# Optimization experiments

Hardware: AMD Instinct MI355X
Metric: run time of the kernel (lower is better)

Reference implementation:

```python
import jax, jax.numpy as jnp
import numpy as np

TEMPERATURE = 2.0  # exp(log(2.0)) clamped to [0.1, 10] -> 2.0
EPS = 1e-8
B, D, P = 2048, 256, 4


def setup_inputs() -> dict:
    key = jax.random.key(0)
    k1, k2, k3, k4 = jax.random.split(key, 4)
    return {
        'z_i': jax.random.normal(k1, (B, D), dtype=jnp.float32),
        'z_j': jax.random.normal(k2, (B, D), dtype=jnp.float32),
        'physics_i': jax.random.uniform(k3, (B, P), dtype=jnp.float32),
        'physics_j': jax.random.uniform(k4, (B, P), dtype=jnp.float32),
    }


def _offdiag(x, flat_idx, n):
    # extract off-diagonal entries of (n,n) -> (n, n-1), row-major order
    return jnp.take(x.reshape(-1), flat_idx).reshape(n, n - 1)


def reference(z_i, z_j, physics_i, physics_j):
    features = jnp.concatenate([z_i, z_j], axis=0)          # (n, D)
    labels = jnp.concatenate([physics_i, physics_j], axis=0)  # (n, P)
    n = features.shape[0]

    # pairwise L1 label distances (n, n)
    label_diffs = jnp.abs(labels[:, None, :] - labels[None, :, :]).sum(-1)

    # cosine similarity logits (n, n)
    f = features / jnp.linalg.norm(features, axis=-1, keepdims=True)
    logits = (f @ f.T) / TEMPERATURE
    logits = logits - jax.lax.stop_gradient(jnp.max(logits, axis=1, keepdims=True))
    exp_logits = jnp.exp(logits)

    flat_idx = jnp.asarray(np.flatnonzero(~np.eye(n, dtype=bool)))
    logits_o = _offdiag(logits, flat_idx, n)      # (n, n-1)
    exp_o = _offdiag(exp_logits, flat_idx, n)
    ld_o = _offdiag(label_diffs, flat_idx, n)

    # denom[i,k] = sum_j [ld_o[i,j] >= ld_o[i,k]] * exp_o[i,j]
    # computed via per-row sort + cumsum instead of the O(n^3) mask loop
    order = jnp.argsort(ld_o, axis=1)
    ld_sorted = jnp.take_along_axis(ld_o, order, axis=1)
    exp_sorted = jnp.take_along_axis(exp_o, order, axis=1)
    csum = jnp.cumsum(exp_sorted, axis=1)
    total = csum[:, -1:]
    # rank[i,k] = number of j with ld_o[i,j] < ld_o[i,k]  (side='left' handles ties)
    rank = jax.vmap(lambda s, q: jnp.searchsorted(s, q, side='left'))(ld_sorted, ld_o)
    below = jnp.where(rank > 0,
                      jnp.take_along_axis(csum, jnp.maximum(rank - 1, 0), axis=1),
                      0.0)
    denom = total - below                          # (n, n-1)

    pos_log_probs = logits_o - jnp.log(denom + EPS)
    loss = -pos_log_probs.sum() / (n * (n - 1))
    return loss
```

## Files before the change

kernel.cpp:

```cpp
#include <hip/hip_runtime.h>
#include <float.h>
#include <math.h>

#define B_SZ   2048
#define D_DIM  256
#define P_DIM  4
#define N_TOT  4096
#define EPS_F  1e-8f
#define RPP    16
#define NBK    512
#define BSCALE 128.0f
#define FIXS   1048576.0f

typedef float     f32x4 __attribute__((ext_vector_type(4)));
typedef long long i64;

__global__ __launch_bounds__(64) void normalize_kernel(
    const float* __restrict__ z_i, const float* __restrict__ z_j,
    unsigned char* __restrict__ fbq)
{
    int row  = blockIdx.x;
    int lane = threadIdx.x;
    const float* src = (row < B_SZ) ? (z_i + (size_t)row * D_DIM)
                                    : (z_j + (size_t)(row - B_SZ) * D_DIM);
    float4 v = ((const float4*)src)[lane];
    float ss = v.x*v.x + v.y*v.y + v.z*v.z + v.w*v.w;
    #pragma unroll
    for (int off = 32; off > 0; off >>= 1)
        ss += __shfl_down(ss, off, 64);
    ss = __shfl(ss, 0, 64);
    float inv = 1.0f / sqrtf(ss);
    int p = __builtin_amdgcn_cvt_pk_fp8_f32(v.x * inv, v.y * inv, 0, false);
    p     = __builtin_amdgcn_cvt_pk_fp8_f32(v.z * inv, v.w * inv, p, true);
    ((int*)(fbq + (size_t)row * D_DIM))[lane] = p;
}

__global__ __launch_bounds__(1024, 4) void panel_kernel(
    const unsigned char* __restrict__ fbq,
    const float* __restrict__ physics_i, const float* __restrict__ physics_j,
    float* __restrict__ partial)
{
    __shared__ unsigned long long hist[RPP * NBK];
    __shared__ float scr[16];

    int tid = threadIdx.x;
    int L   = tid & 63;
    int w   = tid >> 6;
    int i0  = blockIdx.x * RPP;

    uint4 zu = {0u, 0u, 0u, 0u};
    #pragma unroll
    for (int t = 0; t < 4; ++t)
        ((uint4*)hist)[tid + t * 1024] = zu;

    i64 a8[8];
    {
        const unsigned char* ap = fbq + (size_t)(i0 + (L & 15)) * D_DIM + (L >> 4) * 8;
        #pragma unroll
        for (int kc = 0; kc < 8; ++kc)
            a8[kc] = *(const i64*)(ap + kc * 32);
    }
    float4 Lr[4];
    #pragma unroll
    for (int q = 0; q < 4; ++q) {
        int r = i0 + (L >> 4) * 4 + q;
        const float* p = (r < B_SZ) ? physics_i + (size_t)r * P_DIM
                                    : physics_j + (size_t)(r - B_SZ) * P_DIM;
        Lr[q] = *(const float4*)p;
    }

    __syncthreads();

    #define LOADB(BB, LJ, ct)                                                     \
        {                                                                         \
            int jc_ = (ct) * 256 + w * 16 + (L & 15);                             \
            const unsigned char* bp_ = fbq + (size_t)jc_ * D_DIM + (L >> 4) * 8;  \
            _Pragma("unroll")                                                     \
            for (int kc = 0; kc < 8; ++kc)                                        \
                BB[kc] = *(const i64*)(bp_ + kc * 32);                            \
            const float* pj_ = (jc_ < B_SZ)                                       \
                ? physics_i + (size_t)jc_ * P_DIM                                 \
                : physics_j + (size_t)(jc_ - B_SZ) * P_DIM;                       \
            LJ = *(const float4*)pj_;                                             \
        }

    #define COMPUTE(BB, LJ, ct)                                                   \
        {                                                                         \
            int jc_ = (ct) * 256 + w * 16 + (L & 15);                             \
            f32x4 acc0 = {0.f, 0.f, 0.f, 0.f};                                    \
            f32x4 acc1 = {0.f, 0.f, 0.f, 0.f};                                    \
            _Pragma("unroll")                                                     \
            for (int kc = 0; kc < 4; ++kc) {                                      \
                acc0 = __builtin_amdgcn_mfma_f32_16x16x32_fp8_fp8(                \
                    a8[2*kc],   BB[2*kc],   acc0, 0, 0, 0);                       \
                acc1 = __builtin_amdgcn_mfma_f32_16x16x32_fp8_fp8(                \
                    a8[2*kc+1], BB[2*kc+1], acc1, 0, 0, 0);                       \
            }                                                                     \
            _Pragma("unroll")                                                     \
            for (int q = 0; q < 4; ++q) {                                         \
                int rq = (L >> 4) * 4 + q;                                        \
                float logit = (acc0[q] + acc1[q]) * 0.5f;              \
                float d = fabsf(Lr[q].x - LJ.x) + fabsf(Lr[q].y - LJ.y)           \
                        + fabsf(Lr[q].z - LJ.z) + fabsf(Lr[q].w - LJ.w);          \
                int bk = (int)(d * BSCALE); if (bk > NBK - 1) bk = NBK - 1;       \
                if (jc_ != i0 + rq) {                                             \
                    unsigned long long upd = (1ULL << 40)                         \
                        + (unsigned long long)(__expf(logit) * FIXS);             \
                    atomicAdd(&hist[rq * NBK + bk], upd);                         \
                    SL += logit;                                                  \
                }                                                                 \
            }                                                                     \
        }

    float SL = 0.f;
    i64    bA[8], bB[8];
    float4 LjA, LjB;
    LOADB(bA, LjA, 0)
    for (int ct = 0; ct < 16; ct += 2) {
        LOADB(bB, LjB, ct + 1)
        COMPUTE(bA, LjA, ct)
        if (ct + 2 < 16) LOADB(bA, LjA, ct + 2)
        COMPUTE(bB, LjB, ct + 1)
    }
    __syncthreads();

    float term = 0.f;
    {
        const unsigned long long* hr = hist + w * NBK + L * 8;
        float    v[8];
        unsigned c[8];
        float fs = 0.f;
        #pragma unroll
        for (int k = 0; k < 8; ++k) {
            unsigned long long x = hr[k];
            v[k] = (float)(x & 0xFFFFFFFFFFULL) * (1.0f / FIXS);
            c[k] = (unsigned)(x >> 40);
            fs += v[k];
        }
        float s = fs;
        #pragma unroll
        for (int off = 1; off < 64; off <<= 1) {
            float u = __shfl_down(s, off, 64);
            if (L + off < 64) s += u;
        }
        float run = s - fs;
        #pragma unroll
        for (int k = 7; k >= 0; --k) {
            run += v[k];
            if (c[k]) term += (float)c[k] * __logf(run + EPS_F);
        }
    }

    float acc = SL - term;
    #pragma unroll
    for (int off = 32; off > 0; off >>= 1)
        acc += __shfl_down(acc, off, 64);
    if (L == 0) scr[w] = acc;
    __syncthreads();
    if (tid == 0) {
        float s = 0.f;
        #pragma unroll
        for (int w2 = 0; w2 < 16; ++w2) s += scr[w2];
        partial[blockIdx.x] = s;
    }
    #undef LOADB
    #undef COMPUTE
}

__global__ __launch_bounds__(256) void final_kernel(
    const float* __restrict__ partial, float* __restrict__ out)
{
    __shared__ float red[4];
    int tid = threadIdx.x;
    float s = 0.f;
    for (int i = tid; i < N_TOT / RPP; i += 256) s += partial[i];
    #pragma unroll
    for (int off = 32; off > 0; off >>= 1)
        s += __shfl_down(s, off, 64);
    if ((tid & 63) == 0) red[tid >> 6] = s;
    __syncthreads();
    if (tid == 0) {
        double tot = (double)red[0] + red[1] + red[2] + red[3];
        out[0] = (float)(-tot / ((double)N_TOT * (N_TOT - 1)));
    }
}

extern "C" void kernel_launch(void* const* d_in, const int* in_sizes, int n_in,
                              void* d_out, int out_size, void* d_ws, size_t ws_size,
                              hipStream_t stream)
{
    const float* z_i  = (const float*)d_in[0];
    const float* z_j  = (const float*)d_in[1];
    const float* ph_i = (const float*)d_in[2];
    const float* ph_j = (const float*)d_in[3];

    unsigned char* fbq     = (unsigned char*)d_ws;
    float*         partial = (float*)(fbq + (size_t)N_TOT * D_DIM);

    normalize_kernel<<<N_TOT, 64, 0, stream>>>(z_i, z_j, fbq);
    panel_kernel<<<N_TOT / RPP, 1024, 0, stream>>>(fbq, ph_i, ph_j, partial);
    final_kernel<<<1, 256, 0, stream>>>(partial, (float*)d_out);
}
```

Before: 129.1 us.

## Use float LDS histogram and recompute logits in a second pass

The 64-bit fixed-point LDS histogram that packed counts and exp sums is replaced with a 32-bit float histogram updated by float atomics. The suffix sums are written back into the histogram, and a second full pass recomputes the MFMA logits and bucket indices so each pair can look up its denominator and accumulate logit minus log. This removes the 64-bit atomics and halves LDS use, at the cost of doubling the MFMA work and the global B-tile loads and of taking one log per pair instead of one per bucket.

```diff
diff --git a/kernel.cpp b/kernel.cpp
--- a/kernel.cpp
+++ b/kernel.cpp
@@ -10,7 +10,6 @@
 #define RPP    16
 #define NBK    512
 #define BSCALE 128.0f
-#define FIXS   1048576.0f
 
 typedef float     f32x4 __attribute__((ext_vector_type(4)));
 typedef long long i64;
@@ -40,7 +39,7 @@
     const float* __restrict__ physics_i, const float* __restrict__ physics_j,
     float* __restrict__ partial)
 {
-    __shared__ unsigned long long hist[RPP * NBK];
+    __shared__ float hist[RPP * NBK];
     __shared__ float scr[16];
 
     int tid = threadIdx.x;
@@ -48,10 +47,10 @@
     int w   = tid >> 6;
     int i0  = blockIdx.x * RPP;
 
-    uint4 zu = {0u, 0u, 0u, 0u};
-    #pragma unroll
-    for (int t = 0; t < 4; ++t)
-        ((uint4*)hist)[tid + t * 1024] = zu;
+    float4 z4 = {0.f, 0.f, 0.f, 0.f};
+    #pragma unroll
+    for (int t = 0; t < 2; ++t)
+        ((float4*)hist)[tid + t * 1024] = z4;
 
     i64 a8[8];
     {
@@ -84,9 +83,7 @@
             LJ = *(const float4*)pj_;                                             \
         }
 
-    #define COMPUTE(BB, LJ, ct)                                                   \
-        {                                                                         \
-            int jc_ = (ct) * 256 + w * 16 + (L & 15);                             \
+    #define MFMA8(BB)                                                             \
             f32x4 acc0 = {0.f, 0.f, 0.f, 0.f};                                    \
             f32x4 acc1 = {0.f, 0.f, 0.f, 0.f};                                    \
             _Pragma("unroll")                                                     \
@@ -95,7 +92,12 @@
                     a8[2*kc],   BB[2*kc],   acc0, 0, 0, 0);                       \
                 acc1 = __builtin_amdgcn_mfma_f32_16x16x32_fp8_fp8(                \
                     a8[2*kc+1], BB[2*kc+1], acc1, 0, 0, 0);                       \
-            }                                                                     \
+            }
+
+    #define COMPUTE_H(BB, LJ, ct)                                                 \
+        {                                                                         \
+            int jc_ = (ct) * 256 + w * 16 + (L & 15);                             \
+            MFMA8(BB)                                                             \
             _Pragma("unroll")                                                     \
             for (int q = 0; q < 4; ++q) {                                         \
                 int rq = (L >> 4) * 4 + q;                                        \
@@ -103,40 +105,46 @@
                 float d = fabsf(Lr[q].x - LJ.x) + fabsf(Lr[q].y - LJ.y)           \
                         + fabsf(Lr[q].z - LJ.z) + fabsf(Lr[q].w - LJ.w);          \
                 int bk = (int)(d * BSCALE); if (bk > NBK - 1) bk = NBK - 1;       \
-                if (jc_ != i0 + rq) {                                             \
-                    unsigned long long upd = (1ULL << 40)                         \
-                        + (unsigned long long)(__expf(logit) * FIXS);             \
-                    atomicAdd(&hist[rq * NBK + bk], upd);                         \
-                    SL += logit;                                                  \
-                }                                                                 \
+                if (jc_ != i0 + rq)                                               \
+                    atomicAdd(&hist[rq * NBK + bk], __expf(logit));               \
             }                                                                     \
         }
 
-    float SL = 0.f;
-    i64    bA[8], bB[8];
-    float4 LjA, LjB;
-    LOADB(bA, LjA, 0)
-    for (int ct = 0; ct < 16; ct += 2) {
-        LOADB(bB, LjB, ct + 1)
-        COMPUTE(bA, LjA, ct)
-        if (ct + 2 < 16) LOADB(bA, LjA, ct + 2)
-        COMPUTE(bB, LjB, ct + 1)
-    }
-    __syncthreads();
-
-    float term = 0.f;
-    {
-        const unsigned long long* hr = hist + w * NBK + L * 8;
-        float    v[8];
-        unsigned c[8];
+    #define COMPUTE_L(BB, LJ, ct)                                                 \
+        {                                                                         \
+            int jc_ = (ct) * 256 + w * 16 + (L & 15);                             \
+            MFMA8(BB)                                                             \
+            _Pragma("unroll")                                                     \
+            for (int q = 0; q < 4; ++q) {                                         \
+                int rq = (L >> 4) * 4 + q;                                        \
+                float logit = (acc0[q] + acc1[q]) * 0.5f;              \
+                float d = fabsf(Lr[q].x - LJ.x) + fabsf(Lr[q].y - LJ.y)           \
+                        + fabsf(Lr[q].z - LJ.z) + fabsf(Lr[q].w - LJ.w);          \
+                int bk = (int)(d * BSCALE); if (bk > NBK - 1) bk = NBK - 1;       \
+                if (jc_ != i0 + rq)                                               \
+                    ACC += logit - __logf(hist[rq * NBK + bk] + EPS_F);           \
+            }                                                                     \
+        }
+
+    {
+        i64    bA[8], bB[8];
+        float4 LjA, LjB;
+        LOADB(bA, LjA, 0)
+        for (int ct = 0; ct < 16; ct += 2) {
+            LOADB(bB, LjB, ct + 1)
+            COMPUTE_H(bA, LjA, ct)
+            if (ct + 2 < 16) LOADB(bA, LjA, ct + 2)
+            COMPUTE_H(bB, LjB, ct + 1)
+        }
+    }
+    __syncthreads();
+
+    {
+        float* hrow = hist + w * NBK + L * 8;
+        float v[8];
         float fs = 0.f;
         #pragma unroll
-        for (int k = 0; k < 8; ++k) {
-            unsigned long long x = hr[k];
-            v[k] = (float)(x & 0xFFFFFFFFFFULL) * (1.0f / FIXS);
-            c[k] = (unsigned)(x >> 40);
-            fs += v[k];
-        }
+        for (int k = 0; k < 8; ++k) { v[k] = hrow[k]; fs += v[k]; }
         float s = fs;
         #pragma unroll
         for (int off = 1; off < 64; off <<= 1) {
@@ -145,17 +153,27 @@
         }
         float run = s - fs;
         #pragma unroll
-        for (int k = 7; k >= 0; --k) {
-            run += v[k];
-            if (c[k]) term += (float)c[k] * __logf(run + EPS_F);
-        }
-    }
-
-    float acc = SL - term;
+        for (int k = 7; k >= 0; --k) { run += v[k]; hrow[k] = run; }
+    }
+    __syncthreads();
+
+    float ACC = 0.f;
+    {
+        i64    bA[8], bB[8];
+        float4 LjA, LjB;
+        LOADB(bA, LjA, 0)
+        for (int ct = 0; ct < 16; ct += 2) {
+            LOADB(bB, LjB, ct + 1)
+            COMPUTE_L(bA, LjA, ct)
+            if (ct + 2 < 16) LOADB(bA, LjA, ct + 2)
+            COMPUTE_L(bB, LjB, ct + 1)
+        }
+    }
+
     #pragma unroll
     for (int off = 32; off > 0; off >>= 1)
-        acc += __shfl_down(acc, off, 64);
-    if (L == 0) scr[w] = acc;
+        ACC += __shfl_down(ACC, off, 64);
+    if (L == 0) scr[w] = ACC;
     __syncthreads();
     if (tid == 0) {
         float s = 0.f;
@@ -164,7 +182,9 @@
         partial[blockIdx.x] = s;
     }
     #undef LOADB
-    #undef COMPUTE
+    #undef MFMA8
+    #undef COMPUTE_H
+    #undef COMPUTE_L
 }
 
 __global__ __launch_bounds__(256) void final_kernel(
```

Result: slower. 216.2 us (+67.5%).
